# Performance work log

Measured on AMD Instinct MI355X. Metric: run time of the kernel, lower is better.

The kernel has to match this reference:

```python
import jax, jax.numpy as jnp
import numpy as np

B, T, D, H, FF = 4, 2048, 768, 12, 4
DH = D // H


def _ln(x, g, b, eps=1e-5):
    mu = x.mean(-1, keepdims=True)
    var = ((x - mu) ** 2).mean(-1, keepdims=True)
    return (x - mu) * jax.lax.rsqrt(var + eps) * g + b


def setup_inputs() -> dict:
    key = jax.random.key(0)
    ks = jax.random.split(key, 16)
    s = 0.02
    d = {
        'x': jax.random.normal(ks[0], (B, T, D), jnp.float32),
        'Wq': jax.random.normal(ks[1], (D, D), jnp.float32) * s,
        'bq': jnp.zeros((D,), jnp.float32),
        'Wk': jax.random.normal(ks[2], (D, D), jnp.float32) * s,
        'bk': jnp.zeros((D,), jnp.float32),
        'Wv': jax.random.normal(ks[3], (D, D), jnp.float32) * s,
        'bv': jnp.zeros((D,), jnp.float32),
        'Wo': jax.random.normal(ks[4], (D, D), jnp.float32) * s,
        'bo': jnp.zeros((D,), jnp.float32),
        'W1': jax.random.normal(ks[5], (D, D * FF), jnp.float32) * s,
        'b1': jnp.zeros((D * FF,), jnp.float32),
        'W2': jax.random.normal(ks[6], (D * FF, D), jnp.float32) * s,
        'b2': jnp.zeros((D,), jnp.float32),
        'g1': jnp.ones((D,), jnp.float32),
        'be1': jnp.zeros((D,), jnp.float32),
        'g2': jnp.ones((D,), jnp.float32),
        'be2': jnp.zeros((D,), jnp.float32),
        'radius': 64,
    }
    return d


def reference(x, Wq, bq, Wk, bk, Wv, bv, Wo, bo, W1, b1, W2, b2, g1, be1, g2, be2, radius):
    Bc, Tc, Dc = x.shape
    # local mask: blocked (True) where |i-j| > radius (clamping in torch code is a no-op)
    i = jnp.arange(Tc)
    mask = jnp.abs(i[:, None] - i[None, :]) > radius  # [T,T] True = masked

    h = _ln(x, g1, be1)
    q = (h @ Wq + bq).reshape(Bc, Tc, H, DH)
    k = (h @ Wk + bk).reshape(Bc, Tc, H, DH)
    v = (h @ Wv + bv).reshape(Bc, Tc, H, DH)
    scale = 1.0 / jnp.sqrt(jnp.asarray(DH, x.dtype))
    scores = jnp.einsum('bthd,bshd->bhts', q, k) * scale  # [B,H,T,T]
    scores = jnp.where(mask[None, None], -jnp.inf, scores)
    attn = jax.nn.softmax(scores, axis=-1)
    ctx = jnp.einsum('bhts,bshd->bthd', attn, v).reshape(Bc, Tc, Dc)
    x = x + (ctx @ Wo + bo)

    h2 = _ln(x, g2, be2)
    ff = jax.nn.gelu(h2 @ W1 + b1, approximate=False) @ W2 + b2
    return x + ff
```

## Files before the change

### kernel.cpp

```cpp
#include <hip/hip_runtime.h>
#include <hip/hip_bf16.h>

#define B_  4
#define T_  2048
#define D_  768
#define H_  12
#define DH_ 64
#define FF_ 3072

typedef __attribute__((ext_vector_type(8))) short bf16x8;
typedef __attribute__((ext_vector_type(4))) float f32x4;
typedef __attribute__((ext_vector_type(4))) unsigned short us4;

#define MFMA16(a, b, c) __builtin_amdgcn_mfma_f32_16x16x32_bf16((a), (b), (c), 0, 0, 0)

__device__ __forceinline__ unsigned short f2bf(float f) {
    union { float f; unsigned u; } v; v.f = f;
    unsigned r = v.u + 0x7fffu + ((v.u >> 16) & 1u);
    return (unsigned short)(r >> 16);
}

__device__ __forceinline__ void gload_lds16(const unsigned short* gp, unsigned short* lp) {
    __builtin_amdgcn_global_load_lds(
        (const __attribute__((address_space(1))) unsigned int*)gp,
        (__attribute__((address_space(3))) unsigned int*)lp,
        16, 0, 0);
}

__global__ __launch_bounds__(256) void tcvt_kernel(
    const float* __restrict__ src, unsigned short* __restrict__ dst, int K, int N)
{
    __shared__ float tile[32][33];
    const int bx = blockIdx.x * 32;
    const int by = blockIdx.y * 32;
    const int tx = threadIdx.x, ty = threadIdx.y;
#pragma unroll
    for (int i = 0; i < 32; i += 8)
        tile[ty + i][tx] = src[(size_t)(by + ty + i) * N + bx + tx];
    __syncthreads();
#pragma unroll
    for (int i = 0; i < 32; i += 8)
        dst[(size_t)(bx + ty + i) * K + by + tx] = f2bf(tile[tx][ty + i]);
}

__global__ __launch_bounds__(256) void tcvt4_kernel(
    const float* __restrict__ s0, const float* __restrict__ s1,
    const float* __restrict__ s2, const float* __restrict__ s3,
    unsigned short* __restrict__ dst)
{
    __shared__ float tile[32][33];
    const int z = blockIdx.z;
    const float* src = (z == 0) ? s0 : (z == 1) ? s1 : (z == 2) ? s2 : s3;
    unsigned short* d = dst + (size_t)z * 589824;
    const int bx = blockIdx.x * 32;
    const int by = blockIdx.y * 32;
    const int tx = threadIdx.x, ty = threadIdx.y;
#pragma unroll
    for (int i = 0; i < 32; i += 8)
        tile[ty + i][tx] = src[(size_t)(by + ty + i) * 768 + bx + tx];
    __syncthreads();
#pragma unroll
    for (int i = 0; i < 32; i += 8)
        d[(size_t)(bx + ty + i) * 768 + by + tx] = f2bf(tile[tx][ty + i]);
}

__global__ __launch_bounds__(256) void ln_kernel(
    const float* __restrict__ x, const float* __restrict__ g,
    const float* __restrict__ be, unsigned short* __restrict__ out)
{
    const int row = blockIdx.x;
    const int t = threadIdx.x;
    const float* xr = x + (size_t)row * D_;
    float v0 = xr[t], v1 = xr[t + 256], v2 = xr[t + 512];
    float s = v0 + v1 + v2;
    float s2 = v0 * v0 + v1 * v1 + v2 * v2;
#pragma unroll
    for (int o = 1; o < 64; o <<= 1) {
        s  += __shfl_xor(s,  o);
        s2 += __shfl_xor(s2, o);
    }
    __shared__ float rs[4], rq[4];
    const int wave = t >> 6;
    if ((t & 63) == 0) { rs[wave] = s; rq[wave] = s2; }
    __syncthreads();
    s  = rs[0] + rs[1] + rs[2] + rs[3];
    s2 = rq[0] + rq[1] + rq[2] + rq[3];
    const float mu = s * (1.0f / D_);
    const float var = s2 * (1.0f / D_) - mu * mu;
    const float rstd = rsqrtf(var + 1e-5f);
    unsigned short* orow = out + (size_t)row * D_;
    orow[t]       = f2bf((v0 - mu) * rstd * g[t]       + be[t]);
    orow[t + 256] = f2bf((v1 - mu) * rstd * g[t + 256] + be[t + 256]);
    orow[t + 512] = f2bf((v2 - mu) * rstd * g[t + 512] + be[t + 512]);
}

template<int MODE>
__global__ __launch_bounds__(512) void gemm512(
    const unsigned short* __restrict__ A,
    const unsigned short* __restrict__ Bt,
    const float* __restrict__ bias,
    const float* __restrict__ bias2,
    const float* __restrict__ bias3,
    const float* __restrict__ resid,
    void* __restrict__ outp,
    void* __restrict__ out2,
    void* __restrict__ out3,
    int N, int K, int nTilesN)
{
    __shared__ __align__(16) unsigned short As[128 * 64];
    __shared__ __align__(16) unsigned short Bs[128 * 64];

    const int nwg = gridDim.x;
    const int q = nwg >> 3, rr = nwg & 7;
    const int xcd = blockIdx.x & 7, loc = blockIdx.x >> 3;
    const int swz = (xcd < rr ? xcd * (q + 1) : rr * (q + 1) + (xcd - rr) * q) + loc;
    const int m0 = (swz / nTilesN) * 128;
    const int n0 = (swz % nTilesN) * 128;

    const int tid = threadIdx.x;
    const int wv = tid >> 6;
    const int lane = tid & 63;
    const int wr = wv >> 1;
    const int wc = wv & 1;

    f32x4 zero4 = {0.0f, 0.0f, 0.0f, 0.0f};
    f32x4 acc[2][4];
#pragma unroll
    for (int i = 0; i < 2; ++i)
#pragma unroll
        for (int j = 0; j < 4; ++j) acc[i][j] = zero4;

    const int lrow = lane >> 3;
    const int scb = (lane & 7) ^ lrow;
    const size_t ag0 = (size_t)(m0 + wv * 16 + lrow) * K + scb * 8;
    const size_t ag1 = ag0 + (size_t)8 * K;
    const size_t bg0 = (size_t)(n0 + wv * 16 + lrow) * K + scb * 8;
    const size_t bg1 = bg0 + (size_t)8 * K;
    unsigned short* AsW = As + wv * 1024;
    unsigned short* BsW = Bs + wv * 1024;

    const int fr = lane & 15;
    const int fg = lane >> 4;
    const int sw = fr & 7;

    const int nk = K >> 6;
    for (int kt = 0; kt < nk; ++kt) {
        const int k0 = kt << 6;
        __syncthreads();
        gload_lds16(A  + ag0 + k0, AsW);
        gload_lds16(A  + ag1 + k0, AsW + 512);
        gload_lds16(Bt + bg0 + k0, BsW);
        gload_lds16(Bt + bg1 + k0, BsW + 512);
        __syncthreads();
#pragma unroll
        for (int kk = 0; kk < 2; ++kk) {
            bf16x8 afr[2], bfr[4];
#pragma unroll
            for (int mm = 0; mm < 2; ++mm) {
                const int row = wr * 32 + mm * 16 + fr;
                afr[mm] = *(const bf16x8*)(As + row * 64 + (((kk * 4 + fg) ^ sw) << 3));
            }
#pragma unroll
            for (int nn = 0; nn < 4; ++nn) {
                const int row = wc * 64 + nn * 16 + fr;
                bfr[nn] = *(const bf16x8*)(Bs + row * 64 + (((kk * 4 + fg) ^ sw) << 3));
            }
#pragma unroll
            for (int mm = 0; mm < 2; ++mm)
#pragma unroll
                for (int nn = 0; nn < 4; ++nn)
                    acc[mm][nn] = MFMA16(afr[mm], bfr[nn], acc[mm][nn]);
        }
    }

    const int lc = lane & 15;
    const int lr = (lane >> 4) * 4;
#pragma unroll
    for (int mm = 0; mm < 2; ++mm) {
        const int gm0 = m0 + wr * 32 + mm * 16 + lr;
#pragma unroll
        for (int nn = 0; nn < 4; ++nn) {
            const int gn = n0 + wc * 64 + nn * 16 + lc;
            if (MODE == 4) {
                if (gn < 1536) {
                    const float bv = (gn < 768) ? bias[gn] : bias2[gn - 768];
                    unsigned short* o = (gn < 768) ? (unsigned short*)outp : (unsigned short*)out2;
                    const int col = (gn < 768) ? gn : gn - 768;
#pragma unroll
                    for (int r = 0; r < 4; ++r)
                        o[(size_t)(gm0 + r) * 768 + col] = f2bf(acc[mm][nn][r] + bv);
                } else {
                    const float bv = bias3[gn - 1536];
                    const int b = gm0 / T_;
                    const int tl = gm0 - b * T_;
                    us4 pk;
#pragma unroll
                    for (int r = 0; r < 4; ++r) pk[r] = f2bf(acc[mm][nn][r] + bv);
                    *(us4*)((unsigned short*)out3 + ((size_t)(b * D_ + gn - 1536)) * T_ + tl) = pk;
                }
            } else {
                const float bv = bias[gn];
#pragma unroll
                for (int r = 0; r < 4; ++r) {
                    const int gm = gm0 + r;
                    float v = acc[mm][nn][r] + bv;
                    if (MODE == 0) {
                        ((unsigned short*)outp)[(size_t)gm * N + gn] = f2bf(v);
                    } else if (MODE == 2) {
                        v = 0.5f * v * (1.0f + erff(v * 0.70710678118654752f));
                        ((unsigned short*)outp)[(size_t)gm * N + gn] = f2bf(v);
                    } else if (MODE == 3) {
                        ((float*)outp)[(size_t)gm * N + gn] = v + resid[(size_t)gm * N + gn];
                    }
                }
            }
        }
    }
}

__global__ __launch_bounds__(256) void attn_kernel(
    const unsigned short* __restrict__ Q,
    const unsigned short* __restrict__ Kg,
    const unsigned short* __restrict__ Vt,
    unsigned short* __restrict__ ctx)
{
    __shared__ __align__(16) unsigned short Qs[64][72];
    __shared__ __align__(16) unsigned short KP[192 * 72];
    __shared__ __align__(16) unsigned short Vts[64][200];

    const int tid = threadIdx.x;
    const int lane = tid & 63;
    const int w = tid >> 6;
    const int bid = blockIdx.x;
    const int qt = bid & 31;
    const int h = (bid >> 5) % H_;
    const int b = bid / (32 * H_);
    const int qs = qt * 64;
    const int t0 = qs >= 64 ? qs - 64 : 0;
    const int t1 = (qs + 128 < T_) ? qs + 128 : T_;
    const int KW = t1 - t0;

    for (int s = tid; s < 512; s += 256) {
        const int r = s >> 3, c8 = (s & 7) << 3;
        *(uint4*)&Qs[r][c8] =
            *(const uint4*)&Q[((size_t)(b * T_ + qs + r)) * D_ + h * DH_ + c8];
    }
    unsigned short* Ks = KP;
    for (int s = tid; s < 1536; s += 256) {
        const int r = s >> 3, c8 = (s & 7) << 3;
        uint4 val = {0, 0, 0, 0};
        if (r < KW)
            val = *(const uint4*)&Kg[((size_t)(b * T_ + t0 + r)) * D_ + h * DH_ + c8];
        *(uint4*)&Ks[r * 72 + c8] = val;
    }
    for (int s = tid; s < 1536; s += 256) {
        const int r = s / 24, c8 = (s % 24) << 3;
        uint4 val = {0, 0, 0, 0};
        if (c8 < KW)
            val = *(const uint4*)&Vt[((size_t)((b * H_ + h) * DH_ + r)) * T_ + t0 + c8];
        *(uint4*)&Vts[r][c8] = val;
    }
    __syncthreads();

    f32x4 zero4 = {0.0f, 0.0f, 0.0f, 0.0f};
    f32x4 sa[12];
#pragma unroll
    for (int i = 0; i < 12; ++i) sa[i] = zero4;
#pragma unroll
    for (int ks = 0; ks < 2; ++ks) {
        const bf16x8 aq = *(const bf16x8*)&Qs[w * 16 + (lane & 15)][ks * 32 + (lane >> 4) * 8];
#pragma unroll
        for (int cf = 0; cf < 12; ++cf) {
            const bf16x8 bk = *(const bf16x8*)&Ks[(cf * 16 + (lane & 15)) * 72 + ks * 32 + (lane >> 4) * 8];
            sa[cf] = MFMA16(aq, bk, sa[cf]);
        }
    }
    __syncthreads();

    const int lq = w * 16 + (lane >> 4) * 4;
    float mx[4] = {-1e30f, -1e30f, -1e30f, -1e30f};
#pragma unroll
    for (int cf = 0; cf < 12; ++cf) {
        const int key = t0 + cf * 16 + (lane & 15);
#pragma unroll
        for (int r = 0; r < 4; ++r) {
            const int dd = (qs + lq + r) - key;
            const bool ok = (key < t1) && (dd <= 64) && (dd >= -64);
            const float sv = ok ? sa[cf][r] * 0.125f : -1e30f;
            sa[cf][r] = sv;
            mx[r] = fmaxf(mx[r], sv);
        }
    }
#pragma unroll
    for (int r = 0; r < 4; ++r)
#pragma unroll
        for (int o = 1; o < 16; o <<= 1)
            mx[r] = fmaxf(mx[r], __shfl_xor(mx[r], o));

    unsigned short* Ps = KP;
    float sm[4] = {0.0f, 0.0f, 0.0f, 0.0f};
#pragma unroll
    for (int cf = 0; cf < 12; ++cf) {
#pragma unroll
        for (int r = 0; r < 4; ++r) {
            const float p = __expf(sa[cf][r] - mx[r]);
            sm[r] += p;
            Ps[(lq + r) * 200 + cf * 16 + (lane & 15)] = f2bf(p);
        }
    }
#pragma unroll
    for (int r = 0; r < 4; ++r)
#pragma unroll
        for (int o = 1; o < 16; o <<= 1)
            sm[r] += __shfl_xor(sm[r], o);

    f32x4 oa[4];
#pragma unroll
    for (int i = 0; i < 4; ++i) oa[i] = zero4;
#pragma unroll
    for (int ks = 0; ks < 6; ++ks) {
        const bf16x8 ap = *(const bf16x8*)&Ps[(w * 16 + (lane & 15)) * 200 + ks * 32 + (lane >> 4) * 8];
#pragma unroll
        for (int nf = 0; nf < 4; ++nf) {
            const bf16x8 bv = *(const bf16x8*)&Vts[nf * 16 + (lane & 15)][ks * 32 + (lane >> 4) * 8];
            oa[nf] = MFMA16(ap, bv, oa[nf]);
        }
    }
#pragma unroll
    for (int nf = 0; nf < 4; ++nf) {
#pragma unroll
        for (int r = 0; r < 4; ++r) {
            const float o = oa[nf][r] / sm[r];
            ctx[((size_t)(b * T_ + qs + lq + r)) * D_ + h * DH_ + nf * 16 + (lane & 15)] = f2bf(o);
        }
    }
}

extern "C" void kernel_launch(void* const* d_in, const int* in_sizes, int n_in,
                              void* d_out, int out_size, void* d_ws, size_t ws_size,
                              hipStream_t stream)
{
    const float* x   = (const float*)d_in[0];
    const float* Wq  = (const float*)d_in[1];
    const float* bq  = (const float*)d_in[2];
    const float* Wk  = (const float*)d_in[3];
    const float* bk  = (const float*)d_in[4];
    const float* Wv  = (const float*)d_in[5];
    const float* bv  = (const float*)d_in[6];
    const float* Wo  = (const float*)d_in[7];
    const float* bo  = (const float*)d_in[8];
    const float* W1  = (const float*)d_in[9];
    const float* b1  = (const float*)d_in[10];
    const float* W2  = (const float*)d_in[11];
    const float* b2  = (const float*)d_in[12];
    const float* g1  = (const float*)d_in[13];
    const float* be1 = (const float*)d_in[14];
    const float* g2  = (const float*)d_in[15];
    const float* be2 = (const float*)d_in[16];
    float* out = (float*)d_out;

    unsigned short* wqkv_t = (unsigned short*)d_ws;
    unsigned short* wo_t = wqkv_t + 3 * 589824;
    unsigned short* w1_t = wo_t + 589824;
    unsigned short* w2_t = w1_t + 2359296;
    unsigned short* hbuf = w2_t + 2359296;
    unsigned short* qbuf = hbuf + 6291456;
    float* x2 = (float*)(qbuf + 6291456);
    unsigned short* kbuf = (unsigned short*)(x2 + 6291456);
    unsigned short* vtb  = kbuf + 6291456;
    unsigned short* ffb  = kbuf;

    dim3 tb(32, 8);
    tcvt4_kernel<<<dim3(24, 24, 4), tb, 0, stream>>>(Wq, Wk, Wv, Wo, wqkv_t);
    tcvt_kernel<<<dim3(96, 24), tb, 0, stream>>>(W1, w1_t, 768, 3072);
    tcvt_kernel<<<dim3(24, 96), tb, 0, stream>>>(W2, w2_t, 3072, 768);

    ln_kernel<<<8192, 256, 0, stream>>>(x, g1, be1, hbuf);

    gemm512<4><<<64 * 18, 512, 0, stream>>>(
        hbuf, wqkv_t, bq, bk, bv, nullptr, qbuf, kbuf, vtb, 2304, 768, 18);

    attn_kernel<<<1536, 256, 0, stream>>>(qbuf, kbuf, vtb, hbuf);

    gemm512<3><<<64 * 6, 512, 0, stream>>>(
        hbuf, wo_t, bo, nullptr, nullptr, x, x2, nullptr, nullptr, 768, 768, 6);

    ln_kernel<<<8192, 256, 0, stream>>>(x2, g2, be2, qbuf);

    gemm512<2><<<64 * 24, 512, 0, stream>>>(
        qbuf, w1_t, b1, nullptr, nullptr, nullptr, ffb, nullptr, nullptr, 3072, 768, 24);

    gemm512<3><<<64 * 6, 512, 0, stream>>>(
        ffb, w2_t, b2, nullptr, nullptr, x2, out, nullptr, nullptr, 768, 3072, 6);
}
```

Before: 232.9 us.

## Split-K the N=768 GEMMs and fuse partial reduction with bias, residual and LayerNorm

The Wo and W2 projections now run as split-K GEMMs with two K halves. Each half writes its own bf16 partial-sum buffer, which doubles the workgroup count so the 384-tile grids fill the CUs more evenly. A new reduce_ln kernel sums the partials, adds bias and residual, and applies the second LayerNorm in one pass, replacing the separate LN launch. A vectorised reduce_out kernel produces the final output. The cost is extra global traffic for the partial buffers and two extra bf16 roundings of the partial sums, which lowers accuracy.

```diff
diff --git a/kernel.cpp b/kernel.cpp
--- a/kernel.cpp
+++ b/kernel.cpp
@@ -18,6 +18,10 @@
     union { float f; unsigned u; } v; v.f = f;
     unsigned r = v.u + 0x7fffu + ((v.u >> 16) & 1u);
     return (unsigned short)(r >> 16);
+}
+__device__ __forceinline__ float bf2f(unsigned short s) {
+    union { unsigned u; float f; } v; v.u = ((unsigned)s) << 16;
+    return v.f;
 }
 
 __device__ __forceinline__ void gload_lds16(const unsigned short* gp, unsigned short* lp) {
@@ -94,6 +98,66 @@
     orow[t + 512] = f2bf((v2 - mu) * rstd * g[t + 512] + be[t + 512]);
 }
 
+__global__ __launch_bounds__(256) void reduce_ln_kernel(
+    const unsigned short* __restrict__ p0, const unsigned short* __restrict__ p1,
+    const float* __restrict__ x, const float* __restrict__ bo,
+    const float* __restrict__ g, const float* __restrict__ be,
+    float* __restrict__ x2, unsigned short* __restrict__ h2)
+{
+    const int row = blockIdx.x;
+    const int t = threadIdx.x;
+    const size_t base = (size_t)row * D_;
+    float v[3];
+    float s = 0.0f, s2 = 0.0f;
+#pragma unroll
+    for (int j = 0; j < 3; ++j) {
+        const int c = t + j * 256;
+        const float vv = bf2f(p0[base + c]) + bf2f(p1[base + c]) + bo[c] + x[base + c];
+        v[j] = vv;
+        x2[base + c] = vv;
+        s += vv; s2 += vv * vv;
+    }
+#pragma unroll
+    for (int o = 1; o < 64; o <<= 1) {
+        s  += __shfl_xor(s,  o);
+        s2 += __shfl_xor(s2, o);
+    }
+    __shared__ float rs[4], rq[4];
+    const int wave = t >> 6;
+    if ((t & 63) == 0) { rs[wave] = s; rq[wave] = s2; }
+    __syncthreads();
+    s  = rs[0] + rs[1] + rs[2] + rs[3];
+    s2 = rq[0] + rq[1] + rq[2] + rq[3];
+    const float mu = s * (1.0f / D_);
+    const float var = s2 * (1.0f / D_) - mu * mu;
+    const float rstd = rsqrtf(var + 1e-5f);
+#pragma unroll
+    for (int j = 0; j < 3; ++j) {
+        const int c = t + j * 256;
+        h2[base + c] = f2bf((v[j] - mu) * rstd * g[c] + be[c]);
+    }
+}
+
+__global__ __launch_bounds__(256) void reduce_out_kernel(
+    const unsigned short* __restrict__ p0, const unsigned short* __restrict__ p1,
+    const float* __restrict__ x2, const float* __restrict__ b2,
+    float* __restrict__ out)
+{
+    const int n4 = B_ * T_ * D_ / 4;
+    for (int i = blockIdx.x * 256 + threadIdx.x; i < n4; i += gridDim.x * 256) {
+        const us4 a = ((const us4*)p0)[i];
+        const us4 b = ((const us4*)p1)[i];
+        const float4 xr = ((const float4*)x2)[i];
+        const int col = (i * 4) % D_;
+        float4 o;
+        o.x = bf2f(a[0]) + bf2f(b[0]) + b2[col]     + xr.x;
+        o.y = bf2f(a[1]) + bf2f(b[1]) + b2[col + 1] + xr.y;
+        o.z = bf2f(a[2]) + bf2f(b[2]) + b2[col + 2] + xr.z;
+        o.w = bf2f(a[3]) + bf2f(b[3]) + b2[col + 3] + xr.w;
+        ((float4*)out)[i] = o;
+    }
+}
+
 template<int MODE>
 __global__ __launch_bounds__(512) void gemm512(
     const unsigned short* __restrict__ A,
@@ -101,11 +165,10 @@
     const float* __restrict__ bias,
     const float* __restrict__ bias2,
     const float* __restrict__ bias3,
-    const float* __restrict__ resid,
     void* __restrict__ outp,
     void* __restrict__ out2,
     void* __restrict__ out3,
-    int N, int K, int nTilesN)
+    int N, int K, int kLen, int nTilesN, int nTilesMN, long partStride)
 {
     __shared__ __align__(16) unsigned short As[128 * 64];
     __shared__ __align__(16) unsigned short Bs[128 * 64];
@@ -114,8 +177,11 @@
     const int q = nwg >> 3, rr = nwg & 7;
     const int xcd = blockIdx.x & 7, loc = blockIdx.x >> 3;
     const int swz = (xcd < rr ? xcd * (q + 1) : rr * (q + 1) + (xcd - rr) * q) + loc;
-    const int m0 = (swz / nTilesN) * 128;
-    const int n0 = (swz % nTilesN) * 128;
+    const int ks  = swz / nTilesMN;
+    const int rem = swz - ks * nTilesMN;
+    const int m0 = (rem / nTilesN) * 128;
+    const int n0 = (rem % nTilesN) * 128;
+    const int kOff = ks * kLen;
 
     const int tid = threadIdx.x;
     const int wv = tid >> 6;
@@ -132,9 +198,9 @@
 
     const int lrow = lane >> 3;
     const int scb = (lane & 7) ^ lrow;
-    const size_t ag0 = (size_t)(m0 + wv * 16 + lrow) * K + scb * 8;
+    const size_t ag0 = (size_t)(m0 + wv * 16 + lrow) * K + kOff + scb * 8;
     const size_t ag1 = ag0 + (size_t)8 * K;
-    const size_t bg0 = (size_t)(n0 + wv * 16 + lrow) * K + scb * 8;
+    const size_t bg0 = (size_t)(n0 + wv * 16 + lrow) * K + kOff + scb * 8;
     const size_t bg1 = bg0 + (size_t)8 * K;
     unsigned short* AsW = As + wv * 1024;
     unsigned short* BsW = Bs + wv * 1024;
@@ -143,7 +209,7 @@
     const int fg = lane >> 4;
     const int sw = fr & 7;
 
-    const int nk = K >> 6;
+    const int nk = kLen >> 6;
     for (int kt = 0; kt < nk; ++kt) {
         const int k0 = kt << 6;
         __syncthreads();
@@ -198,6 +264,11 @@
                     for (int r = 0; r < 4; ++r) pk[r] = f2bf(acc[mm][nn][r] + bv);
                     *(us4*)((unsigned short*)out3 + ((size_t)(b * D_ + gn - 1536)) * T_ + tl) = pk;
                 }
+            } else if (MODE == 5) {
+                unsigned short* o = (unsigned short*)outp + (size_t)ks * partStride;
+#pragma unroll
+                for (int r = 0; r < 4; ++r)
+                    o[(size_t)(gm0 + r) * N + gn] = f2bf(acc[mm][nn][r]);
             } else {
                 const float bv = bias[gn];
 #pragma unroll
@@ -209,8 +280,6 @@
                     } else if (MODE == 2) {
                         v = 0.5f * v * (1.0f + erff(v * 0.70710678118654752f));
                         ((unsigned short*)outp)[(size_t)gm * N + gn] = f2bf(v);
-                    } else if (MODE == 3) {
-                        ((float*)outp)[(size_t)gm * N + gn] = v + resid[(size_t)gm * N + gn];
                     }
                 }
             }
@@ -378,18 +447,25 @@
     ln_kernel<<<8192, 256, 0, stream>>>(x, g1, be1, hbuf);
 
     gemm512<4><<<64 * 18, 512, 0, stream>>>(
-        hbuf, wqkv_t, bq, bk, bv, nullptr, qbuf, kbuf, vtb, 2304, 768, 18);
+        hbuf, wqkv_t, bq, bk, bv, qbuf, kbuf, vtb, 2304, 768, 768, 18, 64 * 18, 0);
 
     attn_kernel<<<1536, 256, 0, stream>>>(qbuf, kbuf, vtb, hbuf);
 
-    gemm512<3><<<64 * 6, 512, 0, stream>>>(
-        hbuf, wo_t, bo, nullptr, nullptr, x, x2, nullptr, nullptr, 768, 768, 6);
-
-    ln_kernel<<<8192, 256, 0, stream>>>(x2, g2, be2, qbuf);
+    gemm512<5><<<64 * 6 * 2, 512, 0, stream>>>(
+        hbuf, wo_t, nullptr, nullptr, nullptr, kbuf, nullptr, nullptr,
+        768, 768, 384, 6, 64 * 6, 6291456);
+
+    reduce_ln_kernel<<<8192, 256, 0, stream>>>(
+        kbuf, kbuf + 6291456, x, bo, g2, be2, x2, qbuf);
 
     gemm512<2><<<64 * 24, 512, 0, stream>>>(
-        qbuf, w1_t, b1, nullptr, nullptr, nullptr, ffb, nullptr, nullptr, 3072, 768, 24);
-
-    gemm512<3><<<64 * 6, 512, 0, stream>>>(
-        ffb, w2_t, b2, nullptr, nullptr, x2, out, nullptr, nullptr, 768, 3072, 6);
-}
+        qbuf, w1_t, b1, nullptr, nullptr, ffb, nullptr, nullptr,
+        3072, 768, 768, 24, 64 * 24, 0);
+
+    gemm512<5><<<64 * 6 * 2, 512, 0, stream>>>(
+        ffb, w2_t, nullptr, nullptr, nullptr, hbuf, nullptr, nullptr,
+        768, 3072, 1536, 6, 64 * 6, 6291456);
+
+    reduce_out_kernel<<<2048, 256, 0, stream>>>(
+        hbuf, hbuf + 6291456, x2, b2, out);
+}
```

Result: slower. 239.5 us (+2.8%).
